# Kernel optimization log

Measured on AMD Instinct MI355X. Metric: run time of the kernel, lower is better.

## Reference

```python
import jax, jax.numpy as jnp
import numpy as np

KERNEL = 3
STRIDE = 1
PADDING = 1


def _extract_patches(x, k, stride, padding, h_out, w_out):
    # x: [B, C, H, W] -> patches [k, k, B, C, h_out, w_out]
    if padding > 0:
        x = jnp.pad(x, ((0, 0), (0, 0), (padding, padding), (padding, padding)))
    rows = []
    for di in range(k):
        cols = []
        for dj in range(k):
            sl = x[:, :, di:di + (h_out - 1) * stride + 1:stride,
                        dj:dj + (w_out - 1) * stride + 1:stride]
            cols.append(sl)
        rows.append(jnp.stack(cols, axis=0))
    return jnp.stack(rows, axis=0)  # [k, k, B, C, h_out, w_out]


def setup_inputs() -> dict:
    key = jax.random.key(0)
    k1, k2 = jax.random.split(key)
    B, C_in, C_out, H, W = 32, 64, 64, 32, 32
    h_out = (H + 2 * PADDING - KERNEL) // STRIDE + 1
    w_out = (W + 2 * PADDING - KERNEL) // STRIDE + 1
    fan_in = C_in * KERNEL ** 2
    x = jax.random.normal(k1, (B, C_in, H, W), dtype=jnp.float32)
    weight = jax.random.normal(
        k2, (h_out, w_out, C_out, C_in, KERNEL, KERNEL), dtype=jnp.float32
    ) / np.sqrt(fan_in).astype(np.float32)
    bias = jnp.zeros((C_out, h_out, w_out), dtype=jnp.float32)
    return {"x": x, "weight": weight, "bias": bias}


def reference(x, weight, bias):
    h_out, w_out = weight.shape[0], weight.shape[1]
    # patches: [k, k, B, C, h_out, w_out]
    patches = _extract_patches(x, KERNEL, STRIDE, PADDING, h_out, w_out)
    # unshared-weight contraction per spatial location
    # weight: [h_out(x), w_out(y), O, C(i), k(k), k(l)]
    out = jnp.einsum('xyoikl,klbixy->boxy', weight, patches)
    return out + bias[None, :, :, :]
```

## Files before the change

### kernel.cpp

```cpp
#include <hip/hip_runtime.h>

#define HH 32
#define WW 32
#define CIN 64
#define COUT 64
#define BATCH 32
#define KTOT 576
#define NPOS 1024
#define KC 32
#define NCHUNK 18
#define WSTRIDE 260

__device__ float g_xT[CIN * 34 * 34 * BATCH];

__global__ void repack_kernel(const float* __restrict__ x) {
    int t = blockIdx.x * blockDim.x + threadIdx.x;
    int b  = t & 31;
    int s  = t >> 5;
    int ww = s % 34;
    int s2 = s / 34;
    int hh = s2 % 34;
    int i  = s2 / 34;
    float v = 0.f;
    int hs = hh - 1, ws = ww - 1;
    if (hs >= 0 && hs < HH && ws >= 0 && ws < WW)
        v = x[(((b << 6) + i) << 10) + (hs << 5) + ws];
    g_xT[t] = v;
}

__device__ __forceinline__ void async16(const void* src, void* dst_lds) {
    __builtin_amdgcn_global_load_lds(
        (const __attribute__((address_space(1))) void*)src,
        (__attribute__((address_space(3))) void*)dst_lds,
        16, 0, 0);
}

__global__ __launch_bounds__(64) void local2d_kernel(
    const float* __restrict__ weight,
    const float* __restrict__ bias,
    float* __restrict__ out)
{
    __shared__ float Wl[2][8 * WSTRIDE];
    __shared__ float Pl[2][KC * BATCH];

    const int l    = threadIdx.x;
    const int lrow = l >> 3, lcol = l & 7;
    const int og   = l & 7,  bg   = l >> 3;

    int bid = blockIdx.x;
    int xcd = bid & 7;
    int t   = bid >> 3;
    int m   = t & 15;
    int gq  = t >> 4;
    int p   = ((gq << 3) + xcd) * 16 + m;
    int y   = p >> 5, xw = p & 31;

    const float* wpos  = weight + (long)p * (COUT * KTOT);
    const float* wsrc0 = wpos + lrow * KTOT + (lcol << 2);

    float acc[8][4];
#pragma unroll
    for (int a = 0; a < 8; ++a)
#pragma unroll
        for (int c = 0; c < 4; ++c) acc[a][c] = 0.f;

    auto stage = [&](int c, int bsel) {
        const float* ws = wsrc0 + c * KC;
#pragma unroll
        for (int g = 0; g < 8; ++g)
            async16(ws + g * (8 * KTOT), &Wl[bsel][g * WSTRIDE]);
#pragma unroll
        for (int q = 0; q < 4; ++q) {
            int k  = c * KC + (q << 3) + lrow;
            int i  = k / 9;
            int r  = k - i * 9;
            int kh = r / 3;
            int kw = r - kh * 3;
            const float* ps =
                &g_xT[(((i * 34) + y + kh) * 34 + xw + kw) * BATCH + (lcol << 2)];
            async16(ps, &Pl[bsel][q * (8 * BATCH)]);
        }
    };

    auto compute = [&](int bsel) {
        const float* Wb = &Wl[bsel][og * WSTRIDE];
        const float* Pb = &Pl[bsel][bg << 2];
#pragma unroll
        for (int kk = 0; kk < KC; kk += 4) {
            float4 pr[4];
#pragma unroll
            for (int j = 0; j < 4; ++j)
                pr[j] = *(const float4*)(Pb + (kk + j) * BATCH);
            const float* prf = (const float*)pr;
#pragma unroll
            for (int oo = 0; oo < 8; ++oo) {
                float4 wr = *(const float4*)(Wb + oo * 32 + kk);
#pragma unroll
                for (int bb = 0; bb < 4; ++bb) {
                    float a = acc[oo][bb];
                    a = fmaf(wr.x, prf[0 * 4 + bb], a);
                    a = fmaf(wr.y, prf[1 * 4 + bb], a);
                    a = fmaf(wr.z, prf[2 * 4 + bb], a);
                    a = fmaf(wr.w, prf[3 * 4 + bb], a);
                    acc[oo][bb] = a;
                }
            }
        }
    };

    stage(0, 0);
    stage(1, 1);
    for (int c = 0; c < NCHUNK - 1; ++c) {
        asm volatile("s_waitcnt vmcnt(12)" ::: "memory");
        compute(c & 1);
        if (c + 2 < NCHUNK) {
            asm volatile("s_waitcnt lgkmcnt(0)" ::: "memory");
            stage(c + 2, c & 1);
        }
    }
    asm volatile("s_waitcnt vmcnt(0)" ::: "memory");
    compute((NCHUNK - 1) & 1);

#pragma unroll
    for (int oo = 0; oo < 8; ++oo) {
        int o = (og << 3) + oo;
        float bv = bias[(o << 10) + p];
#pragma unroll
        for (int bb = 0; bb < 4; ++bb) {
            int b = (bg << 2) + bb;
            out[(b << 16) + (o << 10) + p] = acc[oo][bb] + bv;
        }
    }
}

extern "C" void kernel_launch(void* const* d_in, const int* in_sizes, int n_in,
                              void* d_out, int out_size, void* d_ws, size_t ws_size,
                              hipStream_t stream) {
    const float* x      = (const float*)d_in[0];
    const float* weight = (const float*)d_in[1];
    const float* bias   = (const float*)d_in[2];
    float* out          = (float*)d_out;

    hipLaunchKernelGGL(repack_kernel, dim3(9248), dim3(256), 0, stream, x);
    hipLaunchKernelGGL(local2d_kernel, dim3(NPOS), dim3(64), 0, stream,
                       weight, bias, out);
}
```

Before: 249.6 us.

## Split K across two waves per block with triple-buffered LDS staging

Each block now runs two wavefronts, and each wave handles half of the 576-long reduction with a 16-wide K chunk. Staging uses three LDS buffers per wave, so the next load is issued before the current chunk is computed. At the end, wave 1 writes its partial sums to LDS and wave 0 adds them, plus the bias, before storing. The aim is more memory-level parallelism and better latency hiding on the weight stream, which is read only once. The cost is a final LDS reduction, a barrier, and higher LDS use per block.

```diff
diff --git a/kernel.cpp b/kernel.cpp
--- a/kernel.cpp
+++ b/kernel.cpp
@@ -7,9 +7,10 @@
 #define BATCH 32
 #define KTOT 576
 #define NPOS 1024
-#define KC 32
-#define NCHUNK 18
-#define WSTRIDE 260
+#define KC 16
+#define KHALF 288
+#define NCW 18
+#define WGRP 260
 
 __device__ float g_xT[CIN * 34 * 34 * BATCH];
 
@@ -35,17 +36,18 @@
         16, 0, 0);
 }
 
-__global__ __launch_bounds__(64) void local2d_kernel(
+__global__ __launch_bounds__(128, 2) void local2d_kernel(
     const float* __restrict__ weight,
     const float* __restrict__ bias,
     float* __restrict__ out)
 {
-    __shared__ float Wl[2][8 * WSTRIDE];
-    __shared__ float Pl[2][KC * BATCH];
+    __shared__ float Wl[2][3][4 * WGRP];
+    __shared__ float Pl[2][3][KC * BATCH];
 
-    const int l    = threadIdx.x;
-    const int lrow = l >> 3, lcol = l & 7;
-    const int og   = l & 7,  bg   = l >> 3;
+    const int wv = threadIdx.x >> 6;
+    const int l  = threadIdx.x & 63;
+
+    const int og = l & 7, bg = l >> 3;
 
     int bid = blockIdx.x;
     int xcd = bid & 7;
@@ -55,8 +57,9 @@
     int p   = ((gq << 3) + xcd) * 16 + m;
     int y   = p >> 5, xw = p & 31;
 
+    const int kbase = wv * KHALF;
     const float* wpos  = weight + (long)p * (COUT * KTOT);
-    const float* wsrc0 = wpos + lrow * KTOT + (lcol << 2);
+    const float* wsrc0 = wpos + (l >> 2) * KTOT + ((l & 3) << 2) + kbase;
 
     float acc[8][4];
 #pragma unroll
@@ -67,24 +70,24 @@
     auto stage = [&](int c, int bsel) {
         const float* ws = wsrc0 + c * KC;
 #pragma unroll
-        for (int g = 0; g < 8; ++g)
-            async16(ws + g * (8 * KTOT), &Wl[bsel][g * WSTRIDE]);
+        for (int g = 0; g < 4; ++g)
+            async16(ws + g * (16 * KTOT), &Wl[wv][bsel][g * WGRP]);
 #pragma unroll
-        for (int q = 0; q < 4; ++q) {
-            int k  = c * KC + (q << 3) + lrow;
+        for (int q = 0; q < 2; ++q) {
+            int k  = kbase + c * KC + (q << 3) + (l >> 3);
             int i  = k / 9;
             int r  = k - i * 9;
             int kh = r / 3;
             int kw = r - kh * 3;
             const float* ps =
-                &g_xT[(((i * 34) + y + kh) * 34 + xw + kw) * BATCH + (lcol << 2)];
-            async16(ps, &Pl[bsel][q * (8 * BATCH)]);
+                &g_xT[(((i * 34) + y + kh) * 34 + xw + kw) * BATCH + ((l & 7) << 2)];
+            async16(ps, &Pl[wv][bsel][q * (8 * BATCH)]);
         }
     };
 
     auto compute = [&](int bsel) {
-        const float* Wb = &Wl[bsel][og * WSTRIDE];
-        const float* Pb = &Pl[bsel][bg << 2];
+        const float* Wb = &Wl[wv][bsel][(og >> 1) * WGRP + ((og & 1) << 3) * 16];
+        const float* Pb = &Pl[wv][bsel][bg << 2];
 #pragma unroll
         for (int kk = 0; kk < KC; kk += 4) {
             float4 pr[4];
@@ -94,7 +97,7 @@
             const float* prf = (const float*)pr;
 #pragma unroll
             for (int oo = 0; oo < 8; ++oo) {
-                float4 wr = *(const float4*)(Wb + oo * 32 + kk);
+                float4 wr = *(const float4*)(Wb + oo * KC + kk);
 #pragma unroll
                 for (int bb = 0; bb < 4; ++bb) {
                     float a = acc[oo][bb];
@@ -110,25 +113,38 @@
 
     stage(0, 0);
     stage(1, 1);
-    for (int c = 0; c < NCHUNK - 1; ++c) {
-        asm volatile("s_waitcnt vmcnt(12)" ::: "memory");
-        compute(c & 1);
-        if (c + 2 < NCHUNK) {
-            asm volatile("s_waitcnt lgkmcnt(0)" ::: "memory");
-            stage(c + 2, c & 1);
+    for (int c = 0; c < NCW - 1; ++c) {
+        asm volatile("s_waitcnt vmcnt(6)" ::: "memory");
+        asm volatile("s_waitcnt lgkmcnt(0)" ::: "memory");
+        if (c + 2 < NCW) stage(c + 2, (c + 2) % 3);
+        compute(c % 3);
+    }
+    asm volatile("s_waitcnt vmcnt(0)" ::: "memory");
+    compute((NCW - 1) % 3);
+
+    __syncthreads();
+    float* R = &Wl[1][0][0];
+    if (wv == 1) {
+#pragma unroll
+        for (int oo = 0; oo < 8; ++oo) {
+            int o = (og << 3) + oo;
+            *(float4*)(&R[o * 36 + (bg << 2)]) =
+                make_float4(acc[oo][0], acc[oo][1], acc[oo][2], acc[oo][3]);
         }
     }
-    asm volatile("s_waitcnt vmcnt(0)" ::: "memory");
-    compute((NCHUNK - 1) & 1);
-
+    __syncthreads();
+    if (wv == 0) {
 #pragma unroll
-    for (int oo = 0; oo < 8; ++oo) {
-        int o = (og << 3) + oo;
-        float bv = bias[(o << 10) + p];
+        for (int oo = 0; oo < 8; ++oo) {
+            int o = (og << 3) + oo;
+            float bv = bias[(o << 10) + p];
+            float4 r = *(const float4*)(&R[o * 36 + (bg << 2)]);
+            const float* rf = (const float*)&r;
 #pragma unroll
-        for (int bb = 0; bb < 4; ++bb) {
-            int b = (bg << 2) + bb;
-            out[(b << 16) + (o << 10) + p] = acc[oo][bb] + bv;
+            for (int bb = 0; bb < 4; ++bb) {
+                int b = (bg << 2) + bb;
+                out[(b << 16) + (o << 10) + p] = acc[oo][bb] + rf[bb] + bv;
+            }
         }
     }
 }
@@ -142,6 +158,6 @@
     float* out          = (float*)d_out;
 
     hipLaunchKernelGGL(repack_kernel, dim3(9248), dim3(256), 0, stream, x);
-    hipLaunchKernelGGL(local2d_kernel, dim3(NPOS), dim3(64), 0, stream,
+    hipLaunchKernelGGL(local2d_kernel, dim3(NPOS), dim3(128), 0, stream,
                        weight, bias, out);
 }
```

New measurement: 246.2 us. About the same (-1.4%).
